# Kernel optimization log

Hardware: AMD Instinct MI355X
Metric: run time of the kernel (lower is better)

The kernel has to match this reference:

```python
import jax, jax.numpy as jnp
import numpy as np

NU, NS, E, M = 200_000, 50_000, 1_000_000, 100_000
FU, FS, H = 64, 64, 128
UIN = 32 + 32 + FU  # user input dim after embedding concat = 128


def setup_inputs() -> dict:
    key = jax.random.key(0)
    ks = jax.random.split(key, 28)
    d = {}
    d["x_user_feat"] = jax.random.normal(ks[0], (NU, FU), jnp.float32)
    d["x_seller_feat"] = jax.random.normal(ks[1], (NS, FS), jnp.float32)
    d["x1"] = jax.random.randint(ks[2], (NU, 2), 0, 3, jnp.int32)  # col0 age<9, col1 gender<3
    d["src_user"] = jax.random.randint(ks[3], (E,), 0, NU, jnp.int32)
    d["dst_seller"] = jax.random.randint(ks[4], (E,), 0, NS, jnp.int32)
    d["src_seller"] = jax.random.randint(ks[5], (E,), 0, NS, jnp.int32)
    d["dst_user"] = jax.random.randint(ks[6], (E,), 0, NU, jnp.int32)
    d["mask_user"] = jax.random.randint(ks[7], (M,), 0, NU, jnp.int32)
    d["mask_seller"] = jax.random.randint(ks[8], (M,), 0, NS, jnp.int32)
    # embeddings
    d["age_emb"] = jax.random.normal(ks[9], (9, 32), jnp.float32)
    d["gen_emb"] = jax.random.normal(ks[10], (3, 32), jnp.float32)
    def w(k, i, o):
        return jax.random.normal(k, (i, o), jnp.float32) / np.sqrt(i).astype(np.float32)
    # layer 1: user update (neighbors are sellers), seller update (neighbors are users)
    d["W1ul"] = w(ks[11], FS, H); d["W1ur"] = w(ks[12], UIN, H); d["b1u"] = jnp.zeros((H,), jnp.float32)
    d["W1sl"] = w(ks[13], UIN, H); d["W1sr"] = w(ks[14], FS, H); d["b1s"] = jnp.zeros((H,), jnp.float32)
    # layer 2
    d["W2ul"] = w(ks[15], H, H); d["W2ur"] = w(ks[16], H, H); d["b2u"] = jnp.zeros((H,), jnp.float32)
    d["W2sl"] = w(ks[17], H, H); d["W2sr"] = w(ks[18], H, H); d["b2s"] = jnp.zeros((H,), jnp.float32)
    d["lin_w"] = w(ks[19], 2 * H, 1); d["lin_b"] = jnp.zeros((1,), jnp.float32)
    return d


def _sage(x_src, x_dst, src, dst, n_dst, Wl, Wr, b):
    # SAGEConv (mean aggr): lin_l(mean_{j in N(i)} x_src[j]) + lin_r(x_dst[i]) + b
    agg = jax.ops.segment_sum(x_src[src], dst, num_segments=n_dst)  # [n_dst, F_src]
    cnt = jax.ops.segment_sum(jnp.ones_like(dst, jnp.float32), dst, num_segments=n_dst)
    mean = agg / jnp.maximum(cnt, 1.0)[:, None]
    return mean @ Wl + x_dst @ Wr + b


def reference(x_user_feat, x_seller_feat, age_emb, gen_emb,
              W1ul, W1ur, b1u, W1sl, W1sr, b1s,
              W2ul, W2ur, b2u, W2sl, W2sr, b2s,
              lin_w, lin_b,
              x1, src_user, dst_seller, src_seller, dst_user,
              mask_user, mask_seller):
    # embedding concat for users
    x_u = jnp.concatenate([age_emb[x1[:, 0]], gen_emb[x1[:, 1]], x_user_feat], axis=1)  # [NU, 128]
    x_s = x_seller_feat  # [NS, 64]
    # layer 1 (HeteroConv aggr='sum' is trivial: one edge type per dst)
    u1 = _sage(x_s, x_u, src_seller, dst_user, NU, W1ul, W1ur, b1u)
    s1 = _sage(x_u, x_s, src_user, dst_seller, NS, W1sl, W1sr, b1s)
    u1, s1 = jax.nn.relu(u1), jax.nn.relu(s1)  # dropout p=0 -> identity
    # layer 2
    u2 = _sage(s1, u1, src_seller, dst_user, NU, W2ul, W2ur, b2u)
    s2 = _sage(u1, s1, src_user, dst_seller, NS, W2sl, W2sr, b2s)
    u2, s2 = jax.nn.relu(u2), jax.nn.relu(s2)
    # mask gather + final linear + sigmoid
    x = jnp.concatenate([u2[mask_user], s2[mask_seller]], axis=1)  # [M, 2H]
    return jax.nn.sigmoid(x @ lin_w + lin_b).reshape(-1)
```

## Files before the change

### kernel.cpp

```cpp
#include <hip/hip_runtime.h>
#include <math.h>

#define NU_N 200000
#define NS_N 50000
#define E_N  1000000
#define M_N  100000
#define NUBG 782
#define NSBG 196

#define CH_E 2048
#define NCH  489
#define NBKT 391
#define CM   191199
#define NCB  747

typedef __attribute__((ext_vector_type(8))) short short8;
typedef __attribute__((ext_vector_type(16))) float f32x16;
typedef unsigned short ushort_t;
typedef unsigned int uint_t;

static constexpr size_t OFF_AGGU  = 0;
static constexpr size_t OFF_AGGS  = 51200000;
static constexpr size_t OFF_U     = 64000000;
static constexpr size_t OFF_S     = 115200256;
static constexpr size_t OFF_XU16  = 128000512;
static constexpr size_t OFF_XS16  = 153600640;
static constexpr size_t OFF_TBL27 = 160000768;
static constexpr size_t OFF_Z1U   = 160014592;
static constexpr size_t OFF_Z1S   = 160047360;
static constexpr size_t OFF_Z2U   = 160084224;
static constexpr size_t OFF_Z2S   = 160149760;
static constexpr size_t OFF_RPU   = 160215296;
static constexpr size_t OFF_RPS   = 161015312;
static constexpr size_t OFF_CSRU  = 161215328;
static constexpr size_t OFF_CSRS  = 165215360;
static constexpr size_t OFF_PART  = 173615392;

static constexpr size_t OFF_TMPU = OFF_AGGU;
static constexpr size_t OFF_TMPS = OFF_AGGU + 8000000;
static constexpr size_t OFF_CMU  = OFF_AGGS;
static constexpr size_t OFF_CMS  = OFF_AGGS + 764800;
static constexpr size_t OFF_CMUS = OFF_AGGS + 1529600;
static constexpr size_t OFF_CMSS = OFF_AGGS + 2294400;

__device__ inline ushort_t f2bf(float f) {
  union { float f; uint_t u; } c; c.f = f;
  uint_t r = (c.u + 0x7FFFu + ((c.u >> 16) & 1u)) >> 16;
  return (ushort_t)r;
}
__device__ inline float u2f(uint_t u) {
  union { uint_t u; float f; } c; c.u = u;
  return c.f;
}
__device__ inline float bf2f(uint_t u) { return u2f(u << 16); }

__global__ void hist_lds_k(const int* __restrict__ du, const int* __restrict__ ds,
                           int* __restrict__ cmatU, int* __restrict__ cmatS) {
  __shared__ int h[NBKT];
  int side = blockIdx.x >= NCH;
  int c = side ? blockIdx.x - NCH : blockIdx.x;
  const int* nd = side ? ds : du;
  int shift = side ? 7 : 9;
  int* cm = side ? cmatS : cmatU;
  for (int i = threadIdx.x; i < NBKT; i += 256) h[i] = 0;
  __syncthreads();
  int e0 = c * CH_E, e1 = min(E_N, e0 + CH_E);
  for (int e = e0 + (int)threadIdx.x; e < e1; e += 256)
    atomicAdd(&h[nd[e] >> shift], 1);
  __syncthreads();
  for (int b = threadIdx.x; b < NBKT; b += 256) cm[b * NCH + c] = h[b];
}

__global__ void scan1_k(const int* __restrict__ cmU, const int* __restrict__ cmS,
                        int* __restrict__ outU, int* __restrict__ outS,
                        int* __restrict__ part) {
  __shared__ int s[256];
  int blk = blockIdx.x;
  const int* in; int* out; int* pp;
  if (blk < NCB) { in = cmU; out = outU; pp = part; }
  else { blk -= NCB; in = cmS; out = outS; pp = part + 1024; }
  int t = threadIdx.x;
  int idx = blk * 256 + t;
  int v = (idx > 0 && idx <= CM) ? in[idx - 1] : 0;
  s[t] = v;
  __syncthreads();
  for (int off = 1; off < 256; off <<= 1) {
    int x = (t >= off) ? s[t - off] : 0;
    __syncthreads();
    s[t] += x;
    __syncthreads();
  }
  if (idx < CM) out[idx] = s[t];
  if (t == 255) pp[blk] = s[255];
}

__global__ void scan2_k(int* __restrict__ part) {
  __shared__ int s[1024];
  int* pp = part + blockIdx.x * 1024;
  int nb = NCB;
  int t = threadIdx.x;
  int v = (t < nb) ? pp[t] : 0;
  s[t] = v;
  __syncthreads();
  for (int off = 1; off < 1024; off <<= 1) {
    int x = (t >= off) ? s[t - off] : 0;
    __syncthreads();
    s[t] += x;
    __syncthreads();
  }
  if (t < nb) pp[t] = s[t] - v;
}

__global__ void scan3_k(int* __restrict__ outU, int* __restrict__ outS,
                        const int* __restrict__ part) {
  int blk = blockIdx.x;
  int* out; const int* pp;
  if (blk < NCB) { out = outU; pp = part; }
  else { blk -= NCB; out = outS; pp = part + 1024; }
  int idx = blk * 256 + threadIdx.x;
  if (idx < CM) out[idx] += pp[blk];
}

__global__ void scatter_k(const int* __restrict__ du, const int* __restrict__ ds,
                          const int* __restrict__ su, const int* __restrict__ ss,
                          const int* __restrict__ cmUs, const int* __restrict__ cmSs,
                          int2* __restrict__ tmpU, int2* __restrict__ tmpS) {
  __shared__ int cur[NBKT];
  int side = blockIdx.x >= NCH;
  int c = side ? blockIdx.x - NCH : blockIdx.x;
  const int* nd = side ? ds : du;
  const int* vv = side ? su : ss;
  const int* cms = side ? cmSs : cmUs;
  int2* tmp = side ? tmpS : tmpU;
  int shift = side ? 7 : 9;
  for (int b = threadIdx.x; b < NBKT; b += 256) cur[b] = cms[b * NCH + c];
  __syncthreads();
  int e0 = c * CH_E, e1 = min(E_N, e0 + CH_E);
  for (int e = e0 + (int)threadIdx.x; e < e1; e += 256) {
    int node = nd[e];
    int pos = atomicAdd(&cur[node >> shift], 1);
    int2 p; p.x = node; p.y = vv[e];
    tmp[pos] = p;
  }
}

__global__ void build_k(const int* __restrict__ cmUs, const int* __restrict__ cmSs,
                        const int2* __restrict__ tmpU, const int2* __restrict__ tmpS,
                        int* __restrict__ rpU, int* __restrict__ rpS,
                        int* __restrict__ csrU, int* __restrict__ csrS) {
  __shared__ int cnt[512];
  __shared__ int s2[256];
  __shared__ int base[512];
  int side = blockIdx.x >= NBKT;
  int b = side ? blockIdx.x - NBKT : blockIdx.x;
  const int* cms = side ? cmSs : cmUs;
  const int2* tmp = side ? tmpS : tmpU;
  int* rp = side ? rpS : rpU;
  int* csr = side ? csrS : csrU;
  int nper = side ? 128 : 512;
  int nn = side ? NS_N : NU_N;
  int t = threadIdx.x;
  int start = cms[b * NCH];
  int end = (b + 1 < NBKT) ? cms[(b + 1) * NCH] : E_N;
  cnt[t] = 0; cnt[t + 256] = 0;
  __syncthreads();
  int nbase = b * nper;
  for (int i = start + t; i < end; i += 256) atomicAdd(&cnt[tmp[i].x - nbase], 1);
  __syncthreads();
  int a0 = cnt[2 * t], a1 = cnt[2 * t + 1];
  s2[t] = a0 + a1;
  __syncthreads();
  int v = s2[t];
  for (int off = 1; off < 256; off <<= 1) {
    int x = (t >= off) ? s2[t - off] : 0;
    __syncthreads();
    s2[t] += x;
    __syncthreads();
  }
  int ex = s2[t] - v;
  base[2 * t] = start + ex;
  base[2 * t + 1] = start + ex + a0;
  __syncthreads();
  for (int i = t; i < nper; i += 256) {
    int node = nbase + i;
    if (node < nn) rp[node] = base[i];
  }
  if (b == NBKT - 1 && t == 0) rp[nn] = E_N;
  __syncthreads();
  for (int i = start + t; i < end; i += 256) {
    int2 p = tmp[i];
    int pos = atomicAdd(&base[p.x - nbase], 1);
    csr[pos] = p.y;
  }
}

__global__ void prep_all_k(const float* __restrict__ xu, const float* __restrict__ xs,
                           const int* __restrict__ x1, const float* __restrict__ age,
                           const float* __restrict__ gen,
                           const float* __restrict__ W1ul, const float* __restrict__ W1ur,
                           const float* __restrict__ W1sl, const float* __restrict__ W1sr,
                           const float* __restrict__ W2ul, const float* __restrict__ W2ur,
                           const float* __restrict__ W2sl, const float* __restrict__ W2sr,
                           ushort_t* __restrict__ xu16, ushort_t* __restrict__ xs16,
                           ushort_t* __restrict__ ub, ushort_t* __restrict__ sb,
                           ushort_t* __restrict__ oh12,
                           float* __restrict__ tbl27,
                           ushort_t* __restrict__ z1u, ushort_t* __restrict__ z1s,
                           ushort_t* __restrict__ z2u, ushort_t* __restrict__ z2s) {
  int t = blockIdx.x * 256 + threadIdx.x;
  if (t < 4000000) {
    const float* src = (t < 3200000) ? xu : xs;
    ushort_t* dst = (t < 3200000) ? xu16 : xs16;
    int i = (t < 3200000) ? t : t - 3200000;
    float4 v = ((const float4*)src)[i];
    uint2 o;
    o.x = (uint_t)f2bf(v.x) | ((uint_t)f2bf(v.y) << 16);
    o.y = (uint_t)f2bf(v.z) | ((uint_t)f2bf(v.w) << 16);
    ((uint2*)dst)[i] = o;
  } else if (t < 4000100) {
    int t3 = t - 4000000;
    uint2 z; z.x = 0u; z.y = 0u;
    if (t3 < 16)       ((uint2*)xu16)[NU_N * 16 + t3] = z;
    else if (t3 < 32)  ((uint2*)xs16)[NS_N * 16 + (t3 - 16)] = z;
    else if (t3 < 64)  ((uint2*)ub)[NU_N * 32 + (t3 - 32)] = z;
    else if (t3 < 96)  ((uint2*)sb)[NS_N * 32 + (t3 - 64)] = z;
    else               ((uint2*)oh12)[NU_N * 4 + (t3 - 96)] = z;
  } else if (t < 4003556) {
    int i = t - 4000100;
    int tt = i >> 7, j = i & 127;
    int a = tt / 3, g = tt % 3;
    float acc = 0.f;
    for (int k = 0; k < 32; ++k) acc += age[a * 32 + k] * W1ur[k * 128 + j];
    for (int k = 0; k < 32; ++k) acc += gen[g * 32 + k] * W1ur[(32 + k) * 128 + j];
    tbl27[i] = acc;
  } else if (t < 4019940) {
    int i = t - 4003556;
    int j = i & 7, lane = (i >> 3) & 63, rest = i >> 9;
    int kt = rest % 8, ct = rest / 8;
    int k = kt * 16 + ((lane >> 5) << 3) + j;
    int n = ct * 32 + (lane & 31);
    float v = (k < 64) ? W1ul[k * 128 + n] : W1ur[k * 128 + n];
    z1u[i] = f2bf(v);
  } else if (t < 4038372) {
    int i = t - 4019940;
    int j = i & 7, lane = (i >> 3) & 63, rest = i >> 9;
    int kt = rest % 9, ct = rest / 9;
    int k = kt * 16 + ((lane >> 5) << 3) + j;
    int n = ct * 32 + (lane & 31);
    float v;
    if (k < 64) v = W1sl[(64 + k) * 128 + n];
    else if (k < 73) {
      int a = k - 64; v = 0.f;
      for (int kk = 0; kk < 32; ++kk) v += age[a * 32 + kk] * W1sl[kk * 128 + n];
    } else if (k < 76) {
      int g = k - 73; v = 0.f;
      for (int kk = 0; kk < 32; ++kk) v += gen[g * 32 + kk] * W1sl[(32 + kk) * 128 + n];
    } else if (k < 80) v = 0.f;
    else v = W1sr[(k - 80) * 128 + n];
    z1s[i] = f2bf(v);
  } else if (t < 4103908) {
    int i = t - 4038372;
    const float *Wl, *Wr; ushort_t* dst;
    if (i < 32768) { Wl = W2ul; Wr = W2ur; dst = z2u; }
    else { Wl = W2sl; Wr = W2sr; dst = z2s; i -= 32768; }
    int j = i & 7, lane = (i >> 3) & 63, rest = i >> 9;
    int kt = rest % 16, ct = rest / 16;
    int k = kt * 16 + ((lane >> 5) << 3) + j;
    int n = ct * 32 + (lane & 31);
    float v = (k < 128) ? Wl[k * 128 + n] : Wr[(k - 128) * 128 + n];
    dst[i] = f2bf(v);
  } else if (t < 4303908) {
    int r = t - 4103908;
    int2 ag = ((const int2*)x1)[r];
    uint_t wds[8];
#pragma unroll
    for (int ww = 0; ww < 8; ++ww) {
      int d0 = 2 * ww, d1 = 2 * ww + 1;
      uint_t lo = ((d0 == ag.x) || (d0 == 9 + ag.y)) ? 0x3F80u : 0u;
      uint_t hi = ((d1 == ag.x) || (d1 == 9 + ag.y)) ? 0x3F80u : 0u;
      wds[ww] = lo | (hi << 16);
    }
    uint4* orow = (uint4*)(oh12 + (size_t)r * 16);
    uint4 o0; o0.x = wds[0]; o0.y = wds[1]; o0.z = wds[2]; o0.w = wds[3];
    uint4 o1; o1.x = wds[4]; o1.y = wds[5]; o1.z = wds[6]; o1.w = wds[7];
    orow[0] = o0;
    orow[1] = o1;
  }
}

#define ACC8(V)                                              \
  acc[0] += bf2f(V.x); acc[1] += u2f(V.x & 0xffff0000u);     \
  acc[2] += bf2f(V.y); acc[3] += u2f(V.y & 0xffff0000u);     \
  acc[4] += bf2f(V.z); acc[5] += u2f(V.z & 0xffff0000u);     \
  acc[6] += bf2f(V.w); acc[7] += u2f(V.w & 0xffff0000u);

template <int R, int R1, int S1STR, int S2STR>
__device__ __forceinline__ void gmeanG(int b, int e, const int* __restrict__ csr,
                                       int zrow, const uint4* __restrict__ src1,
                                       const uint4* __restrict__ src2,
                                       uint4* __restrict__ dst, int c) {
  int n = e - b;
  const uint4* sp; int sstr; int cc;
  if (c < R1) { sp = src1; sstr = S1STR; cc = c; }
  else if (c < R) { sp = src2; sstr = S2STR; cc = c - R1; }
  else { sp = src1; sstr = S1STR; cc = 0; }
  float acc[8];
#pragma unroll
  for (int k = 0; k < 8; ++k) acc[k] = 0.f;
  int j0 = (0 < n) ? csr[b + 0] : zrow;
  int j1 = (1 < n) ? csr[b + 1] : zrow;
  int j2 = (2 < n) ? csr[b + 2] : zrow;
  int j3 = (3 < n) ? csr[b + 3] : zrow;
  uint4 v0 = sp[(size_t)j0 * sstr + cc];
  uint4 v1 = sp[(size_t)j1 * sstr + cc];
  uint4 v2 = sp[(size_t)j2 * sstr + cc];
  uint4 v3 = sp[(size_t)j3 * sstr + cc];
  for (int it = 4; it < n; it += 4) {
    int k0 = csr[b + it];
    int k1 = (it + 1 < n) ? csr[b + it + 1] : zrow;
    int k2 = (it + 2 < n) ? csr[b + it + 2] : zrow;
    int k3 = (it + 3 < n) ? csr[b + it + 3] : zrow;
    uint4 p0 = sp[(size_t)k0 * sstr + cc];
    uint4 p1 = sp[(size_t)k1 * sstr + cc];
    uint4 p2 = sp[(size_t)k2 * sstr + cc];
    uint4 p3 = sp[(size_t)k3 * sstr + cc];
    ACC8(v0); ACC8(v1); ACC8(v2); ACC8(v3);
    v0 = p0; v1 = p1; v2 = p2; v3 = p3;
  }
  ACC8(v0); ACC8(v1); ACC8(v2); ACC8(v3);
  if (c < R) {
    float inv = 1.0f / fmaxf((float)n, 1.0f);
    uint4 o;
    o.x = (uint_t)f2bf(acc[0] * inv) | ((uint_t)f2bf(acc[1] * inv) << 16);
    o.y = (uint_t)f2bf(acc[2] * inv) | ((uint_t)f2bf(acc[3] * inv) << 16);
    o.z = (uint_t)f2bf(acc[4] * inv) | ((uint_t)f2bf(acc[5] * inv) << 16);
    o.w = (uint_t)f2bf(acc[6] * inv) | ((uint_t)f2bf(acc[7] * inv) << 16);
    dst[c] = o;
  }
}

__global__ void gather1_k(const int* __restrict__ rpU, const int* __restrict__ csrU,
                          const ushort_t* __restrict__ xs16,
                          const int* __restrict__ rpS, const int* __restrict__ csrS,
                          const ushort_t* __restrict__ xu16,
                          const ushort_t* __restrict__ oh12,
                          ushort_t* __restrict__ aggU, ushort_t* __restrict__ aggS) {
  int wid = (blockIdx.x * 256 + threadIdx.x) >> 6;
  int lane = threadIdx.x & 63;
  if (wid < 25000) {
    int g = lane >> 3, c = lane & 7;
    int u = wid * 8 + g;
    gmeanG<8, 8, 8, 8>(rpU[u], rpU[u + 1], csrU, NS_N, (const uint4*)xs16,
                       (const uint4*)xs16, (uint4*)(aggU + (size_t)u * 64), c);
  } else {
    int w2 = wid - 25000;
    int g = lane >> 4, c = lane & 15;
    int s = w2 * 4 + g;
    gmeanG<10, 8, 8, 2>(rpS[s], rpS[s + 1], csrS, NU_N, (const uint4*)xu16,
                        (const uint4*)oh12, (uint4*)(aggS + (size_t)s * 80), c);
  }
}

__global__ void gather2_k(const int* __restrict__ rpU, const int* __restrict__ csrU,
                          const ushort_t* __restrict__ s1,
                          const int* __restrict__ rpS, const int* __restrict__ csrS,
                          const ushort_t* __restrict__ u1,
                          ushort_t* __restrict__ aggU, ushort_t* __restrict__ aggS) {
  int wid = (blockIdx.x * 256 + threadIdx.x) >> 6;
  int lane = threadIdx.x & 63;
  int g = lane >> 4, c = lane & 15;
  if (wid < 50000) {
    int u = wid * 4 + g;
    gmeanG<16, 16, 16, 16>(rpU[u], rpU[u + 1], csrU, NS_N, (const uint4*)s1,
                           (const uint4*)s1, (uint4*)(aggU + (size_t)u * 128), c);
  } else {
    int w2 = wid - 50000;
    int s = w2 * 4 + g;
    gmeanG<16, 16, 16, 16>(rpS[s], rpS[s + 1], csrS, NU_N, (const uint4*)u1,
                           (const uint4*)u1, (uint4*)(aggS + (size_t)s * 128), c);
  }
}

template <int KM, int KS, int SSTR, bool TBL>
__device__ __forceinline__ void gemm_core(
    short* sW, int bid, int nrows, const ushort_t* __restrict__ agg,
    const ushort_t* self, const ushort_t* __restrict__ wswz,
    const float* __restrict__ bias, const float* __restrict__ tbl27,
    const int* __restrict__ x1, ushort_t* out) {
  constexpr int K = KM + KS;
  constexpr int NKT = K / 16;
  {
    const uint4* g4 = (const uint4*)wswz;
    uint4* s4 = (uint4*)sW;
    for (int i = threadIdx.x; i < K * 16; i += 256) s4[i] = g4[i];
  }
  __syncthreads();

  int wave = threadIdx.x >> 6, lane = threadIdx.x & 63;
  int r0 = bid * 256 + wave * 64;
  int qk = (lane >> 5) << 3;

  int ra = r0 + (lane & 31), rb = ra + 32;
  int rac = (ra < nrows) ? ra : 0, rbc = (rb < nrows) ? rb : 0;

  f32x16 acc[2][4];
#pragma unroll
  for (int rt = 0; rt < 2; ++rt)
#pragma unroll
    for (int ct = 0; ct < 4; ++ct) acc[rt][ct] = (f32x16)0.0f;

  const short8* sWv = (const short8*)sW;

#pragma unroll
  for (int kt = 0; kt < NKT; ++kt) {
    int k0 = kt * 16 + qk;
    short8 af, bf;
    if (kt * 16 < KM) {
      af = *((const short8*)(agg + (size_t)rac * KM + k0));
      bf = *((const short8*)(agg + (size_t)rbc * KM + k0));
    } else {
      af = *((const short8*)(self + (size_t)rac * SSTR + (k0 - KM)));
      bf = *((const short8*)(self + (size_t)rbc * SSTR + (k0 - KM)));
    }
#pragma unroll
    for (int ct = 0; ct < 4; ++ct) {
      short8 wf = sWv[(ct * NKT + kt) * 64 + lane];
      acc[0][ct] = __builtin_amdgcn_mfma_f32_32x32x16_bf16(af, wf, acc[0][ct], 0, 0, 0);
      acc[1][ct] = __builtin_amdgcn_mfma_f32_32x32x16_bf16(bf, wf, acc[1][ct], 0, 0, 0);
    }
  }

  int nloc = lane & 31;
  float bn[4];
#pragma unroll
  for (int ct = 0; ct < 4; ++ct) bn[ct] = bias[ct * 32 + nloc];
  int rowq = 4 * (lane >> 5);
#pragma unroll
  for (int rt = 0; rt < 2; ++rt) {
#pragma unroll
    for (int reg = 0; reg < 16; ++reg) {
      int row = r0 + rt * 32 + (reg & 3) + 8 * (reg >> 2) + rowq;
      if (row < nrows) {
        const float* tp = nullptr;
        if (TBL) {
          int a = x1[2 * row], g = x1[2 * row + 1];
          tp = tbl27 + (a * 3 + g) * 128 + nloc;
        }
#pragma unroll
        for (int ct = 0; ct < 4; ++ct) {
          float v = acc[rt][ct][reg] + bn[ct];
          if (TBL) v += tp[ct * 32];
          out[(size_t)row * 128 + ct * 32 + nloc] = f2bf(fmaxf(v, 0.0f));
        }
      }
    }
  }
}

__global__ __launch_bounds__(256, 2) void gemm1_k(
    const ushort_t* __restrict__ aggU, const ushort_t* __restrict__ aggS,
    const ushort_t* __restrict__ xu16, const ushort_t* __restrict__ xs16,
    const ushort_t* __restrict__ z1u, const ushort_t* __restrict__ z1s,
    const float* __restrict__ b1u, const float* __restrict__ b1s,
    const float* __restrict__ tbl27, const int* __restrict__ x1,
    ushort_t* __restrict__ ub, ushort_t* __restrict__ sb) {
  extern __shared__ short smem[];
  if (blockIdx.x < NUBG)
    gemm_core<64, 64, 64, true>(smem, blockIdx.x, NU_N, aggU, xu16, z1u, b1u, tbl27, x1, ub);
  else
    gemm_core<80, 64, 64, false>(smem, blockIdx.x - NUBG, NS_N, aggS, xs16, z1s, b1s,
                                 nullptr, nullptr, sb);
}

__global__ __launch_bounds__(256, 2) void gemm2_k(
    const ushort_t* __restrict__ aggU, const ushort_t* __restrict__ aggS,
    const ushort_t* __restrict__ z2u, const ushort_t* __restrict__ z2s,
    const float* __restrict__ b2u, const float* __restrict__ b2s,
    ushort_t* ub, ushort_t* sb) {
  extern __shared__ short smem[];
  if (blockIdx.x < NUBG)
    gemm_core<128, 128, 128, false>(smem, blockIdx.x, NU_N, aggU, ub, z2u, b2u,
                                    nullptr, nullptr, ub);
  else
    gemm_core<128, 128, 128, false>(smem, blockIdx.x - NUBG, NS_N, aggS, sb, z2s, b2s,
                                    nullptr, nullptr, sb);
}

__global__ void final_k(const ushort_t* __restrict__ u2, const ushort_t* __restrict__ s2,
                        const int* __restrict__ mu, const int* __restrict__ ms,
                        const float* __restrict__ lw, const float* __restrict__ lb,
                        float* __restrict__ out) {
  int w = (blockIdx.x * blockDim.x + threadIdx.x) >> 6;
  int lane = threadIdx.x & 63;
  if (w >= M_N) return;
  int iu = mu[w], is = ms[w];
  uint_t a = ((const uint_t*)(u2 + (size_t)iu * 128))[lane];
  uint_t b = ((const uint_t*)(s2 + (size_t)is * 128))[lane];
  float p = bf2f(a & 0xffffu) * lw[2 * lane] + bf2f(a >> 16) * lw[2 * lane + 1]
          + bf2f(b & 0xffffu) * lw[128 + 2 * lane] + bf2f(b >> 16) * lw[129 + 2 * lane];
#pragma unroll
  for (int off = 32; off > 0; off >>= 1) p += __shfl_down(p, off, 64);
  if (lane == 0) out[w] = 1.0f / (1.0f + expf(-(p + lb[0])));
}

extern "C" void kernel_launch(void* const* d_in, const int* in_sizes, int n_in,
                              void* d_out, int out_size, void* d_ws, size_t ws_size,
                              hipStream_t stream) {
  const float* xu   = (const float*)d_in[0];
  const float* xs   = (const float*)d_in[1];
  const int*   x1   = (const int*)d_in[2];
  const int*   su   = (const int*)d_in[3];
  const int*   ds   = (const int*)d_in[4];
  const int*   ss   = (const int*)d_in[5];
  const int*   du   = (const int*)d_in[6];
  const int*   mu   = (const int*)d_in[7];
  const int*   ms   = (const int*)d_in[8];
  const float* age  = (const float*)d_in[9];
  const float* gen  = (const float*)d_in[10];
  const float* W1ul = (const float*)d_in[11];
  const float* W1ur = (const float*)d_in[12];
  const float* b1u  = (const float*)d_in[13];
  const float* W1sl = (const float*)d_in[14];
  const float* W1sr = (const float*)d_in[15];
  const float* b1s  = (const float*)d_in[16];
  const float* W2ul = (const float*)d_in[17];
  const float* W2ur = (const float*)d_in[18];
  const float* b2u  = (const float*)d_in[19];
  const float* W2sl = (const float*)d_in[20];
  const float* W2sr = (const float*)d_in[21];
  const float* b2s  = (const float*)d_in[22];
  const float* lw   = (const float*)d_in[23];
  const float* lb   = (const float*)d_in[24];

  char* w = (char*)d_ws;
  ushort_t* aggU = (ushort_t*)(w + OFF_AGGU);
  ushort_t* aggS = (ushort_t*)(w + OFF_AGGS);
  ushort_t* ub   = (ushort_t*)(w + OFF_U);
  ushort_t* sb   = (ushort_t*)(w + OFF_S);
  ushort_t* xu16 = (ushort_t*)(w + OFF_XU16);
  ushort_t* xs16 = (ushort_t*)(w + OFF_XS16);
  float* tbl27   = (float*)(w + OFF_TBL27);
  ushort_t* z1u  = (ushort_t*)(w + OFF_Z1U);
  ushort_t* z1s  = (ushort_t*)(w + OFF_Z1S);
  ushort_t* z2u  = (ushort_t*)(w + OFF_Z2U);
  ushort_t* z2s  = (ushort_t*)(w + OFF_Z2S);
  int* rpU    = (int*)(w + OFF_RPU);
  int* rpS    = (int*)(w + OFF_RPS);
  int* csrU   = (int*)(w + OFF_CSRU);
  int* csrS   = (int*)(w + OFF_CSRS);
  int2* tmpU  = (int2*)(w + OFF_TMPU);
  int2* tmpS  = (int2*)(w + OFF_TMPS);
  int* cmatU  = (int*)(w + OFF_CMU);
  int* cmatS  = (int*)(w + OFF_CMS);
  int* cmatUs = (int*)(w + OFF_CMUS);
  int* cmatSs = (int*)(w + OFF_CMSS);
  ushort_t* oh12 = (ushort_t*)(w + OFF_U);
  int* part   = (int*)(w + OFF_PART);
  float* out = (float*)d_out;

  hist_lds_k<<<2 * NCH, 256, 0, stream>>>(du, ds, cmatU, cmatS);
  scan1_k<<<2 * NCB, 256, 0, stream>>>(cmatU, cmatS, cmatUs, cmatSs, part);
  scan2_k<<<2, 1024, 0, stream>>>(part);
  scan3_k<<<2 * NCB, 256, 0, stream>>>(cmatUs, cmatSs, part);
  scatter_k<<<2 * NCH, 256, 0, stream>>>(du, ds, su, ss, cmatUs, cmatSs, tmpU, tmpS);
  build_k<<<2 * NBKT, 256, 0, stream>>>(cmatUs, cmatSs, tmpU, tmpS,
                                        rpU, rpS, csrU, csrS);
  prep_all_k<<<16813, 256, 0, stream>>>(xu, xs, x1, age, gen,
                                        W1ul, W1ur, W1sl, W1sr, W2ul, W2ur, W2sl, W2sr,
                                        xu16, xs16, ub, sb, oh12, tbl27,
                                        z1u, z1s, z2u, z2s);

  gather1_k<<<9375, 256, 0, stream>>>(rpU, csrU, xs16, rpS, csrS, xu16, oh12,
                                      aggU, aggS);
  gemm1_k<<<NUBG + NSBG, 256, 144 * 128 * 2, stream>>>(aggU, aggS, xu16, xs16, z1u, z1s,
                                                       b1u, b1s, tbl27, x1, ub, sb);

  gather2_k<<<15625, 256, 0, stream>>>(rpU, csrU, sb, rpS, csrS, ub, aggU, aggS);
  gemm2_k<<<NUBG + NSBG, 256, 256 * 128 * 2, stream>>>(aggU, aggS, z2u, z2s,
                                                       b2u, b2s, ub, sb);

  final_k<<<(M_N * 64 + 255) / 256, 256, 0, stream>>>(ub, sb, mu, ms, lw, lb, out);
}
```

Baseline: 453.1 us.

## Fuse histogram into prep kernel, merge scan phases, use dot2 bf16 accumulate

```diff
diff --git a/kernel.cpp b/kernel.cpp
--- a/kernel.cpp
+++ b/kernel.cpp
@@ -13,6 +13,7 @@
 #define NBKT 391
 #define CM   191199
 #define NCB  747
+#define PREPB 16813
 
 typedef __attribute__((ext_vector_type(8))) short short8;
 typedef __attribute__((ext_vector_type(16))) float f32x16;
@@ -54,160 +55,39 @@
 }
 __device__ inline float bf2f(uint_t u) { return u2f(u << 16); }
 
-__global__ void hist_lds_k(const int* __restrict__ du, const int* __restrict__ ds,
-                           int* __restrict__ cmatU, int* __restrict__ cmatS) {
+__global__ void prep_hist_k(const float* __restrict__ xu, const float* __restrict__ xs,
+                            const int* __restrict__ x1, const float* __restrict__ age,
+                            const float* __restrict__ gen,
+                            const float* __restrict__ W1ul, const float* __restrict__ W1ur,
+                            const float* __restrict__ W1sl, const float* __restrict__ W1sr,
+                            const float* __restrict__ W2ul, const float* __restrict__ W2ur,
+                            const float* __restrict__ W2sl, const float* __restrict__ W2sr,
+                            ushort_t* __restrict__ xu16, ushort_t* __restrict__ xs16,
+                            ushort_t* __restrict__ ub, ushort_t* __restrict__ sb,
+                            ushort_t* __restrict__ oh12,
+                            float* __restrict__ tbl27,
+                            ushort_t* __restrict__ z1u, ushort_t* __restrict__ z1s,
+                            ushort_t* __restrict__ z2u, ushort_t* __restrict__ z2s,
+                            const int* __restrict__ du, const int* __restrict__ ds,
+                            int* __restrict__ cmatU, int* __restrict__ cmatS) {
   __shared__ int h[NBKT];
-  int side = blockIdx.x >= NCH;
-  int c = side ? blockIdx.x - NCH : blockIdx.x;
-  const int* nd = side ? ds : du;
-  int shift = side ? 7 : 9;
-  int* cm = side ? cmatS : cmatU;
-  for (int i = threadIdx.x; i < NBKT; i += 256) h[i] = 0;
-  __syncthreads();
-  int e0 = c * CH_E, e1 = min(E_N, e0 + CH_E);
-  for (int e = e0 + (int)threadIdx.x; e < e1; e += 256)
-    atomicAdd(&h[nd[e] >> shift], 1);
-  __syncthreads();
-  for (int b = threadIdx.x; b < NBKT; b += 256) cm[b * NCH + c] = h[b];
-}
-
-__global__ void scan1_k(const int* __restrict__ cmU, const int* __restrict__ cmS,
-                        int* __restrict__ outU, int* __restrict__ outS,
-                        int* __restrict__ part) {
-  __shared__ int s[256];
-  int blk = blockIdx.x;
-  const int* in; int* out; int* pp;
-  if (blk < NCB) { in = cmU; out = outU; pp = part; }
-  else { blk -= NCB; in = cmS; out = outS; pp = part + 1024; }
-  int t = threadIdx.x;
-  int idx = blk * 256 + t;
-  int v = (idx > 0 && idx <= CM) ? in[idx - 1] : 0;
-  s[t] = v;
-  __syncthreads();
-  for (int off = 1; off < 256; off <<= 1) {
-    int x = (t >= off) ? s[t - off] : 0;
-    __syncthreads();
-    s[t] += x;
-    __syncthreads();
-  }
-  if (idx < CM) out[idx] = s[t];
-  if (t == 255) pp[blk] = s[255];
-}
-
-__global__ void scan2_k(int* __restrict__ part) {
-  __shared__ int s[1024];
-  int* pp = part + blockIdx.x * 1024;
-  int nb = NCB;
-  int t = threadIdx.x;
-  int v = (t < nb) ? pp[t] : 0;
-  s[t] = v;
-  __syncthreads();
-  for (int off = 1; off < 1024; off <<= 1) {
-    int x = (t >= off) ? s[t - off] : 0;
-    __syncthreads();
-    s[t] += x;
-    __syncthreads();
-  }
-  if (t < nb) pp[t] = s[t] - v;
-}
-
-__global__ void scan3_k(int* __restrict__ outU, int* __restrict__ outS,
-                        const int* __restrict__ part) {
-  int blk = blockIdx.x;
-  int* out; const int* pp;
-  if (blk < NCB) { out = outU; pp = part; }
-  else { blk -= NCB; out = outS; pp = part + 1024; }
-  int idx = blk * 256 + threadIdx.x;
-  if (idx < CM) out[idx] += pp[blk];
-}
-
-__global__ void scatter_k(const int* __restrict__ du, const int* __restrict__ ds,
-                          const int* __restrict__ su, const int* __restrict__ ss,
-                          const int* __restrict__ cmUs, const int* __restrict__ cmSs,
-                          int2* __restrict__ tmpU, int2* __restrict__ tmpS) {
-  __shared__ int cur[NBKT];
-  int side = blockIdx.x >= NCH;
-  int c = side ? blockIdx.x - NCH : blockIdx.x;
-  const int* nd = side ? ds : du;
-  const int* vv = side ? su : ss;
-  const int* cms = side ? cmSs : cmUs;
-  int2* tmp = side ? tmpS : tmpU;
-  int shift = side ? 7 : 9;
-  for (int b = threadIdx.x; b < NBKT; b += 256) cur[b] = cms[b * NCH + c];
-  __syncthreads();
-  int e0 = c * CH_E, e1 = min(E_N, e0 + CH_E);
-  for (int e = e0 + (int)threadIdx.x; e < e1; e += 256) {
-    int node = nd[e];
-    int pos = atomicAdd(&cur[node >> shift], 1);
-    int2 p; p.x = node; p.y = vv[e];
-    tmp[pos] = p;
-  }
-}
-
-__global__ void build_k(const int* __restrict__ cmUs, const int* __restrict__ cmSs,
-                        const int2* __restrict__ tmpU, const int2* __restrict__ tmpS,
-                        int* __restrict__ rpU, int* __restrict__ rpS,
-                        int* __restrict__ csrU, int* __restrict__ csrS) {
-  __shared__ int cnt[512];
-  __shared__ int s2[256];
-  __shared__ int base[512];
-  int side = blockIdx.x >= NBKT;
-  int b = side ? blockIdx.x - NBKT : blockIdx.x;
-  const int* cms = side ? cmSs : cmUs;
-  const int2* tmp = side ? tmpS : tmpU;
-  int* rp = side ? rpS : rpU;
-  int* csr = side ? csrS : csrU;
-  int nper = side ? 128 : 512;
-  int nn = side ? NS_N : NU_N;
-  int t = threadIdx.x;
-  int start = cms[b * NCH];
-  int end = (b + 1 < NBKT) ? cms[(b + 1) * NCH] : E_N;
-  cnt[t] = 0; cnt[t + 256] = 0;
-  __syncthreads();
-  int nbase = b * nper;
-  for (int i = start + t; i < end; i += 256) atomicAdd(&cnt[tmp[i].x - nbase], 1);
-  __syncthreads();
-  int a0 = cnt[2 * t], a1 = cnt[2 * t + 1];
-  s2[t] = a0 + a1;
-  __syncthreads();
-  int v = s2[t];
-  for (int off = 1; off < 256; off <<= 1) {
-    int x = (t >= off) ? s2[t - off] : 0;
-    __syncthreads();
-    s2[t] += x;
-    __syncthreads();
-  }
-  int ex = s2[t] - v;
-  base[2 * t] = start + ex;
-  base[2 * t + 1] = start + ex + a0;
-  __syncthreads();
-  for (int i = t; i < nper; i += 256) {
-    int node = nbase + i;
-    if (node < nn) rp[node] = base[i];
-  }
-  if (b == NBKT - 1 && t == 0) rp[nn] = E_N;
-  __syncthreads();
-  for (int i = start + t; i < end; i += 256) {
-    int2 p = tmp[i];
-    int pos = atomicAdd(&base[p.x - nbase], 1);
-    csr[pos] = p.y;
-  }
-}
-
-__global__ void prep_all_k(const float* __restrict__ xu, const float* __restrict__ xs,
-                           const int* __restrict__ x1, const float* __restrict__ age,
-                           const float* __restrict__ gen,
-                           const float* __restrict__ W1ul, const float* __restrict__ W1ur,
-                           const float* __restrict__ W1sl, const float* __restrict__ W1sr,
-                           const float* __restrict__ W2ul, const float* __restrict__ W2ur,
-                           const float* __restrict__ W2sl, const float* __restrict__ W2sr,
-                           ushort_t* __restrict__ xu16, ushort_t* __restrict__ xs16,
-                           ushort_t* __restrict__ ub, ushort_t* __restrict__ sb,
-                           ushort_t* __restrict__ oh12,
-                           float* __restrict__ tbl27,
-                           ushort_t* __restrict__ z1u, ushort_t* __restrict__ z1s,
-                           ushort_t* __restrict__ z2u, ushort_t* __restrict__ z2s) {
-  int t = blockIdx.x * 256 + threadIdx.x;
+  if (blockIdx.x < 2 * NCH) {
+    int bid = blockIdx.x;
+    int side = bid >= NCH;
+    int c = side ? bid - NCH : bid;
+    const int* nd = side ? ds : du;
+    int shift = side ? 7 : 9;
+    int* cm = side ? cmatS : cmatU;
+    for (int i = threadIdx.x; i < NBKT; i += 256) h[i] = 0;
+    __syncthreads();
+    int e0 = c * CH_E, e1 = min(E_N, e0 + CH_E);
+    for (int e = e0 + (int)threadIdx.x; e < e1; e += 256)
+      atomicAdd(&h[nd[e] >> shift], 1);
+    __syncthreads();
+    for (int b = threadIdx.x; b < NBKT; b += 256) cm[b * NCH + c] = h[b];
+    return;
+  }
+  int t = (blockIdx.x - 2 * NCH) * 256 + threadIdx.x;
   if (t < 4000000) {
     const float* src = (t < 3200000) ? xu : xs;
     ushort_t* dst = (t < 3200000) ? xu16 : xs16;
@@ -288,17 +168,138 @@
   }
 }
 
-#define ACC8(V)                                              \
-  acc[0] += bf2f(V.x); acc[1] += u2f(V.x & 0xffff0000u);     \
-  acc[2] += bf2f(V.y); acc[3] += u2f(V.y & 0xffff0000u);     \
-  acc[4] += bf2f(V.z); acc[5] += u2f(V.z & 0xffff0000u);     \
-  acc[6] += bf2f(V.w); acc[7] += u2f(V.w & 0xffff0000u);
+__global__ void scan1_k(const int* __restrict__ cmU, const int* __restrict__ cmS,
+                        int* __restrict__ outU, int* __restrict__ outS,
+                        int* __restrict__ part) {
+  __shared__ int s[256];
+  int blk = blockIdx.x;
+  const int* in; int* out; int* pp;
+  if (blk < NCB) { in = cmU; out = outU; pp = part; }
+  else { blk -= NCB; in = cmS; out = outS; pp = part + 1024; }
+  int t = threadIdx.x;
+  int idx = blk * 256 + t;
+  int v = (idx > 0 && idx <= CM) ? in[idx - 1] : 0;
+  s[t] = v;
+  __syncthreads();
+  for (int off = 1; off < 256; off <<= 1) {
+    int x = (t >= off) ? s[t - off] : 0;
+    __syncthreads();
+    s[t] += x;
+    __syncthreads();
+  }
+  if (idx < CM) out[idx] = s[t];
+  if (t == 255) pp[blk] = s[255];
+}
+
+__global__ void scan3_k(int* __restrict__ outU, int* __restrict__ outS,
+                        const int* __restrict__ part) {
+  __shared__ int red[256];
+  int blk = blockIdx.x;
+  int* out; const int* pp;
+  if (blk < NCB) { out = outU; pp = part; }
+  else { blk -= NCB; out = outS; pp = part + 1024; }
+  int t = threadIdx.x;
+  int s = 0;
+  for (int i = t; i < blk; i += 256) s += pp[i];
+  red[t] = s;
+  __syncthreads();
+  for (int off = 128; off > 0; off >>= 1) {
+    if (t < off) red[t] += red[t + off];
+    __syncthreads();
+  }
+  int off0 = red[0];
+  int idx = blk * 256 + t;
+  if (idx < CM) out[idx] += off0;
+}
+
+__global__ void scatter_k(const int* __restrict__ du, const int* __restrict__ ds,
+                          const int* __restrict__ su, const int* __restrict__ ss,
+                          const int* __restrict__ cmUs, const int* __restrict__ cmSs,
+                          int2* __restrict__ tmpU, int2* __restrict__ tmpS) {
+  __shared__ int cur[NBKT];
+  int side = blockIdx.x >= NCH;
+  int c = side ? blockIdx.x - NCH : blockIdx.x;
+  const int* nd = side ? ds : du;
+  const int* vv = side ? su : ss;
+  const int* cms = side ? cmSs : cmUs;
+  int2* tmp = side ? tmpS : tmpU;
+  int shift = side ? 7 : 9;
+  for (int b = threadIdx.x; b < NBKT; b += 256) cur[b] = cms[b * NCH + c];
+  __syncthreads();
+  int e0 = c * CH_E, e1 = min(E_N, e0 + CH_E);
+  for (int e = e0 + (int)threadIdx.x; e < e1; e += 256) {
+    int node = nd[e];
+    int pos = atomicAdd(&cur[node >> shift], 1);
+    int2 p; p.x = node; p.y = vv[e];
+    tmp[pos] = p;
+  }
+}
+
+__global__ void build_k(const int* __restrict__ cmUs, const int* __restrict__ cmSs,
+                        const int2* __restrict__ tmpU, const int2* __restrict__ tmpS,
+                        int* __restrict__ rpU, int* __restrict__ rpS,
+                        int* __restrict__ csrU, int* __restrict__ csrS) {
+  __shared__ int cnt[512];
+  __shared__ int s2[256];
+  __shared__ int base[512];
+  int side = blockIdx.x >= NBKT;
+  int b = side ? blockIdx.x - NBKT : blockIdx.x;
+  const int* cms = side ? cmSs : cmUs;
+  const int2* tmp = side ? tmpS : tmpU;
+  int* rp = side ? rpS : rpU;
+  int* csr = side ? csrS : csrU;
+  int nper = side ? 128 : 512;
+  int nn = side ? NS_N : NU_N;
+  int t = threadIdx.x;
+  int start = cms[b * NCH];
+  int end = (b + 1 < NBKT) ? cms[(b + 1) * NCH] : E_N;
+  cnt[t] = 0; cnt[t + 256] = 0;
+  __syncthreads();
+  int nbase = b * nper;
+  for (int i = start + t; i < end; i += 256) atomicAdd(&cnt[tmp[i].x - nbase], 1);
+  __syncthreads();
+  int a0 = cnt[2 * t], a1 = cnt[2 * t + 1];
+  s2[t] = a0 + a1;
+  __syncthreads();
+  int v = s2[t];
+  for (int off = 1; off < 256; off <<= 1) {
+    int x = (t >= off) ? s2[t - off] : 0;
+    __syncthreads();
+    s2[t] += x;
+    __syncthreads();
+  }
+  int ex = s2[t] - v;
+  base[2 * t] = start + ex;
+  base[2 * t + 1] = start + ex + a0;
+  __syncthreads();
+  for (int i = t; i < nper; i += 256) {
+    int node = nbase + i;
+    if (node < nn) rp[node] = base[i];
+  }
+  if (b == NBKT - 1 && t == 0) rp[nn] = E_N;
+  __syncthreads();
+  for (int i = start + t; i < end; i += 256) {
+    int2 p = tmp[i];
+    int pos = atomicAdd(&base[p.x - nbase], 1);
+    csr[pos] = p.y;
+  }
+}
+
+__device__ __forceinline__ void dot2acc(float& a, uint_t u, uint_t sel) {
+  asm("v_dot2_f32_bf16 %0, %1, %2, %0" : "+v"(a) : "v"(u), "v"(sel));
+}
+#define DACC8(V)                                             \
+  dot2acc(acc[0], V.x, SEL_LO); dot2acc(acc[1], V.x, SEL_HI);\
+  dot2acc(acc[2], V.y, SEL_LO); dot2acc(acc[3], V.y, SEL_HI);\
+  dot2acc(acc[4], V.z, SEL_LO); dot2acc(acc[5], V.z, SEL_HI);\
+  dot2acc(acc[6], V.w, SEL_LO); dot2acc(acc[7], V.w, SEL_HI);
 
 template <int R, int R1, int S1STR, int S2STR>
 __device__ __forceinline__ void gmeanG(int b, int e, const int* __restrict__ csr,
                                        int zrow, const uint4* __restrict__ src1,
                                        const uint4* __restrict__ src2,
                                        uint4* __restrict__ dst, int c) {
+  const uint_t SEL_LO = 0x00003F80u, SEL_HI = 0x3F800000u;
   int n = e - b;
   const uint4* sp; int sstr; int cc;
   if (c < R1) { sp = src1; sstr = S1STR; cc = c; }
@@ -324,10 +325,10 @@
     uint4 p1 = sp[(size_t)k1 * sstr + cc];
     uint4 p2 = sp[(size_t)k2 * sstr + cc];
     uint4 p3 = sp[(size_t)k3 * sstr + cc];
-    ACC8(v0); ACC8(v1); ACC8(v2); ACC8(v3);
+    DACC8(v0); DACC8(v1); DACC8(v2); DACC8(v3);
     v0 = p0; v1 = p1; v2 = p2; v3 = p3;
   }
-  ACC8(v0); ACC8(v1); ACC8(v2); ACC8(v3);
+  DACC8(v0); DACC8(v1); DACC8(v2); DACC8(v3);
   if (c < R) {
     float inv = 1.0f / fmaxf((float)n, 1.0f);
     uint4 o;
@@ -558,17 +559,16 @@
   int* part   = (int*)(w + OFF_PART);
   float* out = (float*)d_out;
 
-  hist_lds_k<<<2 * NCH, 256, 0, stream>>>(du, ds, cmatU, cmatS);
+  prep_hist_k<<<2 * NCH + PREPB, 256, 0, stream>>>(
+      xu, xs, x1, age, gen, W1ul, W1ur, W1sl, W1sr, W2ul, W2ur, W2sl, W2sr,
+      xu16, xs16, ub, sb, oh12, tbl27, z1u, z1s, z2u, z2s,
+      du, ds, cmatU, cmatS);
+
   scan1_k<<<2 * NCB, 256, 0, stream>>>(cmatU, cmatS, cmatUs, cmatSs, part);
-  scan2_k<<<2, 1024, 0, stream>>>(part);
   scan3_k<<<2 * NCB, 256, 0, stream>>>(cmatUs, cmatSs, part);
   scatter_k<<<2 * NCH, 256, 0, stream>>>(du, ds, su, ss, cmatUs, cmatSs, tmpU, tmpS);
   build_k<<<2 * NBKT, 256, 0, stream>>>(cmatUs, cmatSs, tmpU, tmpS,
                                         rpU, rpS, csrU, csrS);
-  prep_all_k<<<16813, 256, 0, stream>>>(xu, xs, x1, age, gen,
-                                        W1ul, W1ur, W1sl, W1sr, W2ul, W2ur, W2sl, W2sr,
-                                        xu16, xs16, ub, sb, oh12, tbl27,
-                                        z1u, z1s, z2u, z2s);
 
   gather1_k<<<9375, 256, 0, stream>>>(rpU, csrU, xs16, rpS, csrS, xu16, oh12,
                                       aggU, aggS);
```

Measured after the change: 443.0 us (median of 2 runs). -2.2%, faster.
